# Performance work log

Hardware: AMD Instinct MI355X
Metric: run time of the kernel (lower is better)

Reference implementation:

```python
import jax, jax.numpy as jnp
import numpy as np

HID = 2880
NQ = 64
NKV = 8
HD = 64
THETA = 150000.0
WINDOW = 128
S = 8192


def _rope(x, positions):
    # x: [S, H, D]; half-split (rotate_half) convention
    d = x.shape[-1]
    inv_freq = 1.0 / (THETA ** (jnp.arange(0, d, 2, dtype=jnp.float32) / d))  # [D/2]
    ang = positions.astype(jnp.float32)[:, None] * inv_freq[None, :]          # [S, D/2]
    cos = jnp.cos(ang)[:, None, :]
    sin = jnp.sin(ang)[:, None, :]
    x1, x2 = jnp.split(x, 2, axis=-1)
    return jnp.concatenate([x1 * cos - x2 * sin, x2 * cos + x1 * sin], axis=-1)


def setup_inputs() -> dict:
    key = jax.random.key(0)
    ks = jax.random.split(key, 12)
    sd = 0.02
    return {
        "hidden": jax.random.normal(ks[0], (S, HID), dtype=jnp.float32),
        "positions": jnp.arange(S, dtype=jnp.int64) if jax.config.jax_enable_x64 else jnp.arange(S, dtype=jnp.int32),
        "Wq": jax.random.normal(ks[1], (HID, NQ * HD), dtype=jnp.float32) * sd,
        "bq": jax.random.normal(ks[2], (NQ * HD,), dtype=jnp.float32) * sd,
        "Wk": jax.random.normal(ks[3], (HID, NKV * HD), dtype=jnp.float32) * sd,
        "bk": jax.random.normal(ks[4], (NKV * HD,), dtype=jnp.float32) * sd,
        "Wv": jax.random.normal(ks[5], (HID, NKV * HD), dtype=jnp.float32) * sd,
        "bv": jax.random.normal(ks[6], (NKV * HD,), dtype=jnp.float32) * sd,
        "Wo": jax.random.normal(ks[7], (NQ * HD, HID), dtype=jnp.float32) * sd,
        "bo": jax.random.normal(ks[8], (HID,), dtype=jnp.float32) * sd,
    }


def _attention(hidden, positions, Wq, bq, Wk, bk, Wv, bv, Wo, bo):
    n_tok = hidden.shape[0]
    q = (hidden @ Wq + bq).reshape(n_tok, NQ, HD)
    k = (hidden @ Wk + bk).reshape(n_tok, NKV, HD)
    v = (hidden @ Wv + bv).reshape(n_tok, NKV, HD)
    q = _rope(q, positions)
    k = _rope(k, positions)

    # Blocked sliding-window causal attention (window == block size W).
    W = WINDOW
    nb = n_tok // W
    group = NQ // NKV
    qb = q.reshape(nb, W, NQ, HD)
    kb = k.reshape(nb, W, NKV, HD)
    vb = v.reshape(nb, W, NKV, HD)
    # each query block attends to its own block plus the previous one (2W keys)
    k_prev = jnp.concatenate([jnp.zeros_like(kb[:1]), kb[:-1]], axis=0)
    v_prev = jnp.concatenate([jnp.zeros_like(vb[:1]), vb[:-1]], axis=0)
    k_ctx = jnp.concatenate([k_prev, kb], axis=1)   # [nb, 2W, NKV, HD]
    v_ctx = jnp.concatenate([v_prev, vb], axis=1)
    # GQA: repeat KV heads to match query heads
    k_ctx = jnp.repeat(k_ctx, group, axis=2)        # [nb, 2W, NQ, HD]
    v_ctx = jnp.repeat(v_ctx, group, axis=2)

    scale = 1.0 / np.sqrt(HD)
    scores = jnp.einsum('bqhd,bkhd->bhqk', qb, k_ctx) * scale  # [nb, NQ, W, 2W]

    qi = jnp.arange(W)[:, None]            # local query pos
    ki = jnp.arange(2 * W)[None, :]        # local key pos within context
    diff = qi - ki + W                     # i - j (global)
    band = (diff >= 0) & (diff < WINDOW)   # causal + window
    kpos = jnp.arange(nb)[:, None, None] * W + ki[None] - W  # global key pos
    mask = band[None] & (kpos >= 0)        # [nb, W, 2W]

    neg = jnp.finfo(scores.dtype).min
    scores = jnp.where(mask[:, None, :, :], scores, neg)
    p = jax.nn.softmax(scores, axis=-1)
    attn = jnp.einsum('bhqk,bkhd->bqhd', p, v_ctx)  # [nb, W, NQ, HD]
    attn = attn.reshape(n_tok, NQ * HD)
    return attn @ Wo + bo


def reference(hidden, positions, Wq, bq, Wk, bk, Wv, bv, Wo, bo):
    return _attention(hidden, positions, Wq, bq, Wk, bk, Wv, bv, Wo, bo)
```

## Files before the change

kernel.cpp:

```cpp
#include <hip/hip_runtime.h>
#include <stdint.h>

#define S_TOK 8192
#define HID 2880
#define NQ 64
#define NKV 8
#define HD 64
#define QKV_N 5120
#define NO_PAD 2944

typedef __attribute__((ext_vector_type(8))) __bf16 bf16x8;
typedef __attribute__((ext_vector_type(4))) float f32x4;
typedef __attribute__((ext_vector_type(16))) float f32x16;

__device__ __forceinline__ unsigned short f2bf(float f) {
  unsigned int u = __builtin_bit_cast(unsigned int, f);
  u += 0x7fff + ((u >> 16) & 1);
  return (unsigned short)(u >> 16);
}
__device__ __forceinline__ float bf2f(unsigned short h) {
  unsigned int u = ((unsigned int)h) << 16;
  return __builtin_bit_cast(float, u);
}

__device__ __forceinline__ void async_lds16(const void* g, void* l) {
  __builtin_amdgcn_global_load_lds(
      (const __attribute__((address_space(1))) unsigned int*)g,
      (__attribute__((address_space(3))) unsigned int*)l, 16, 0, 0);
}

__global__ __launch_bounds__(256) void cvt_bf16_kernel(
    const float* __restrict__ src, unsigned short* __restrict__ dst) {
  size_t i = ((size_t)blockIdx.x * 256 + threadIdx.x) * 8;
  float4 a = *(const float4*)(src + i);
  float4 b = *(const float4*)(src + i + 4);
  union { unsigned short u[8]; uint4 v; } o;
  o.u[0] = f2bf(a.x); o.u[1] = f2bf(a.y); o.u[2] = f2bf(a.z); o.u[3] = f2bf(a.w);
  o.u[4] = f2bf(b.x); o.u[5] = f2bf(b.y); o.u[6] = f2bf(b.z); o.u[7] = f2bf(b.w);
  *(uint4*)(dst + i) = o.v;
}

__global__ __launch_bounds__(256) void transpose_cvt(
    const float* __restrict__ src, unsigned short* __restrict__ dst,
    int R, int C, int rowOff) {
  __shared__ float tile[32][33];
  int tx = threadIdx.x, ty = threadIdx.y;
  int c0 = blockIdx.x * 32, r0 = blockIdx.y * 32;
#pragma unroll
  for (int i = 0; i < 4; ++i)
    tile[ty + i * 8][tx] = src[(size_t)(r0 + ty + i * 8) * C + c0 + tx];
  __syncthreads();
#pragma unroll
  for (int i = 0; i < 4; ++i)
    dst[(size_t)(c0 + ty + i * 8 + rowOff) * R + r0 + tx] = f2bf(tile[tx][ty + i * 8]);
}

__global__ __launch_bounds__(256) void rope_kernel(
    unsigned short* __restrict__ qkv, const int* __restrict__ positions) {
  int gid = blockIdx.x * 256 + threadIdx.x;
  int d = gid & 31;
  int rest = gid >> 5;
  int head = rest % 72;
  int t = rest / 72;
  unsigned short* p = qkv + (size_t)t * QKV_N + head * 64;
  float x1 = bf2f(p[d]);
  float x2 = bf2f(p[d + 32]);
  float pos = (float)positions[t];
  float inv = exp2f(-0.5373313430f * (float)d);
  float ang = pos * inv;
  float s = sinf(ang), c = cosf(ang);
  p[d] = f2bf(x1 * c - x2 * s);
  p[d + 32] = f2bf(x2 * c + x1 * s);
}

template <int MODE>
__global__ __launch_bounds__(256) void gemm_bt(
    const unsigned short* __restrict__ A, const unsigned short* __restrict__ BT,
    void* __restrict__ Cout, int K,
    const float* __restrict__ b0, const float* __restrict__ b1,
    const float* __restrict__ b2) {
  __shared__ unsigned short lds[128 * 128];
  unsigned short* As = lds;
  unsigned short* Bs = lds + 128 * 64;
  const int tid = threadIdx.x;
  const int wave = tid >> 6, lane = tid & 63;
  const int l31 = lane & 31, lh = lane >> 5;
  const int wy = wave >> 1, wx = wave & 1;
  const int m0 = blockIdx.y * 128, n0 = blockIdx.x * 128;

  f32x16 acc[2][2];
#pragma unroll
  for (int i = 0; i < 2; ++i)
#pragma unroll
    for (int j = 0; j < 2; ++j)
#pragma unroll
      for (int r = 0; r < 16; ++r) acc[i][j][r] = 0.f;

  for (int k0 = 0; k0 < K; k0 += 64) {
    const unsigned short* Ag = A + (size_t)m0 * K + k0;
    const unsigned short* Bg = BT + (size_t)n0 * K + k0;
#pragma unroll
    for (int i = 0; i < 4; ++i) {
      int s = tid + i * 256;
      int row = s >> 3;
      int c = (s & 7) ^ (row & 7);
      async_lds16(Ag + (size_t)row * K + c * 8, &As[s * 8]);
      async_lds16(Bg + (size_t)row * K + c * 8, &Bs[s * 8]);
    }
    __syncthreads();
#pragma unroll
    for (int ks = 0; ks < 4; ++ks) {
      bf16x8 af[2], bfr[2];
#pragma unroll
      for (int ra = 0; ra < 2; ++ra) {
        int row = wy * 64 + ra * 32 + l31;
        int p = (ks * 2 + lh) ^ (row & 7);
        af[ra] = *(const bf16x8*)&As[row * 64 + p * 8];
      }
#pragma unroll
      for (int cb = 0; cb < 2; ++cb) {
        int row = wx * 64 + cb * 32 + l31;
        int p = (ks * 2 + lh) ^ (row & 7);
        bfr[cb] = *(const bf16x8*)&Bs[row * 64 + p * 8];
      }
#pragma unroll
      for (int ra = 0; ra < 2; ++ra)
#pragma unroll
        for (int cb = 0; cb < 2; ++cb)
          acc[ra][cb] = __builtin_amdgcn_mfma_f32_32x32x16_bf16(
              af[ra], bfr[cb], acc[ra][cb], 0, 0, 0);
    }
    __syncthreads();
  }

  if (MODE == 0) {
#pragma unroll
    for (int cb = 0; cb < 2; ++cb) {
      int col = wx * 64 + cb * 32 + l31;
      int gcol = n0 + col;
      float bias = (gcol < 4096) ? b0[gcol]
                                 : (gcol < 4608 ? b1[gcol - 4096] : b2[gcol - 4608]);
#pragma unroll
      for (int ra = 0; ra < 2; ++ra) {
#pragma unroll
        for (int r = 0; r < 16; ++r) {
          int row = wy * 64 + ra * 32 + (r & 3) + 8 * (r >> 2) + 4 * lh;
          lds[row * 128 + col] = f2bf(acc[ra][cb][r] + bias);
        }
      }
    }
    __syncthreads();
    unsigned short* C16 = (unsigned short*)Cout;
#pragma unroll
    for (int i = 0; i < 8; ++i) {
      int s = tid + i * 256;
      int row = s >> 4, cc = (s & 15) * 8;
      *(uint4*)(C16 + (size_t)(m0 + row) * QKV_N + n0 + cc) =
          *(const uint4*)&lds[row * 128 + cc];
    }
  } else {
#pragma unroll
    for (int cb = 0; cb < 2; ++cb) {
      int gcol = n0 + wx * 64 + cb * 32 + l31;
      if (gcol < HID) {
        float bias = b0[gcol];
#pragma unroll
        for (int ra = 0; ra < 2; ++ra) {
#pragma unroll
          for (int r = 0; r < 16; ++r) {
            int row = m0 + wy * 64 + ra * 32 + (r & 3) + 8 * (r >> 2) + 4 * lh;
            ((float*)Cout)[(size_t)row * HID + gcol] = acc[ra][cb][r] + bias;
          }
        }
      }
    }
  }
}

__global__ __launch_bounds__(256) void attn_kernel(
    const unsigned short* __restrict__ qkv, unsigned short* __restrict__ attn) {
  __shared__ unsigned short Qs[64 * 72];
  __shared__ unsigned short Ks[192 * 72];
  __shared__ unsigned short VTs[64 * 200];

  const int tid = threadIdx.x;
  const int B = blockIdx.x;
  const int h = blockIdx.y;
  const int hk = h >> 3;
  const int wave = tid >> 6, lane = tid & 63;
  const int quad = lane >> 4, ml = lane & 15;

#pragma unroll
  for (int it = 0; it < 2; ++it) {
    int s = tid + it * 256;
    int row = s >> 3, c = (s & 7) << 3;
    *(uint4*)&Qs[row * 72 + c] =
        *(const uint4*)(qkv + (size_t)(B * 64 + row) * QKV_N + h * 64 + c);
  }
#pragma unroll
  for (int it = 0; it < 6; ++it) {
    int s = tid + it * 256;
    int j = s >> 3, c = (s & 7) << 3;
    int tk = B * 64 - 128 + j;
    uint4 kv = make_uint4(0, 0, 0, 0), vv = make_uint4(0, 0, 0, 0);
    if (tk >= 0) {
      kv = *(const uint4*)(qkv + (size_t)tk * QKV_N + 4096 + hk * 64 + c);
      vv = *(const uint4*)(qkv + (size_t)tk * QKV_N + 4608 + hk * 64 + c);
    }
    *(uint4*)&Ks[j * 72 + c] = kv;
    union { uint4 q; unsigned short u[8]; } vu;
    vu.q = vv;
#pragma unroll
    for (int e = 0; e < 8; ++e) VTs[(c + e) * 200 + j] = vu.u[e];
  }
  __syncthreads();

  f32x4 zero = {0.f, 0.f, 0.f, 0.f};
  f32x4 sc[12];
#pragma unroll
  for (int jn = 0; jn < 12; ++jn) sc[jn] = zero;
#pragma unroll
  for (int kk = 0; kk < 2; ++kk) {
    bf16x8 af = *(const bf16x8*)&Qs[(wave * 16 + ml) * 72 + kk * 32 + quad * 8];
#pragma unroll
    for (int jn = 0; jn < 12; ++jn) {
      bf16x8 bfr = *(const bf16x8*)&Ks[(jn * 16 + ml) * 72 + kk * 32 + quad * 8];
      sc[jn] = __builtin_amdgcn_mfma_f32_16x16x32_bf16(af, bfr, sc[jn], 0, 0, 0);
    }
  }

  const float NEG = -3.0e38f;
  float mx[4], sm[4];
#pragma unroll
  for (int r = 0; r < 4; ++r) mx[r] = NEG;
#pragma unroll
  for (int jn = 0; jn < 12; ++jn) {
    int j = jn * 16 + ml;
#pragma unroll
    for (int r = 0; r < 4; ++r) {
      int i = wave * 16 + quad * 4 + r;
      bool valid = (j > i) && (j <= i + 128) && (B * 64 + j - 128 >= 0);
      float v = valid ? sc[jn][r] * 0.125f : NEG;
      sc[jn][r] = v;
      mx[r] = fmaxf(mx[r], v);
    }
  }
#pragma unroll
  for (int r = 0; r < 4; ++r) {
#pragma unroll
    for (int off = 1; off < 16; off <<= 1)
      mx[r] = fmaxf(mx[r], __shfl_xor(mx[r], off, 64));
    sm[r] = 0.f;
  }
#pragma unroll
  for (int jn = 0; jn < 12; ++jn) {
#pragma unroll
    for (int r = 0; r < 4; ++r) {
      float p = expf(sc[jn][r] - mx[r]);
      sc[jn][r] = p;
      sm[r] += p;
    }
  }
#pragma unroll
  for (int r = 0; r < 4; ++r) {
#pragma unroll
    for (int off = 1; off < 16; off <<= 1) sm[r] += __shfl_xor(sm[r], off, 64);
    sm[r] = 1.0f / sm[r];
  }
  __syncthreads();

  unsigned short* P = Ks;
#pragma unroll
  for (int jn = 0; jn < 12; ++jn) {
#pragma unroll
    for (int r = 0; r < 4; ++r)
      P[(wave * 16 + quad * 4 + r) * 200 + jn * 16 + ml] = f2bf(sc[jn][r] * sm[r]);
  }
  __syncthreads();

  f32x4 ov[4];
#pragma unroll
  for (int jn = 0; jn < 4; ++jn) ov[jn] = zero;
#pragma unroll
  for (int ks = 0; ks < 6; ++ks) {
    bf16x8 af = *(const bf16x8*)&P[(wave * 16 + ml) * 200 + ks * 32 + quad * 8];
#pragma unroll
    for (int jn = 0; jn < 4; ++jn) {
      bf16x8 bfr = *(const bf16x8*)&VTs[(jn * 16 + ml) * 200 + ks * 32 + quad * 8];
      ov[jn] = __builtin_amdgcn_mfma_f32_16x16x32_bf16(af, bfr, ov[jn], 0, 0, 0);
    }
  }
#pragma unroll
  for (int jn = 0; jn < 4; ++jn) {
#pragma unroll
    for (int r = 0; r < 4; ++r) {
      int row = B * 64 + wave * 16 + quad * 4 + r;
      attn[(size_t)row * 4096 + h * 64 + jn * 16 + ml] = f2bf(ov[jn][r]);
    }
  }
}

extern "C" void kernel_launch(void* const* d_in, const int* in_sizes, int n_in,
                              void* d_out, int out_size, void* d_ws, size_t ws_size,
                              hipStream_t stream) {
  const float* hidden = (const float*)d_in[0];
  const int* positions = (const int*)d_in[1];
  const float* Wq = (const float*)d_in[2];
  const float* bq = (const float*)d_in[3];
  const float* Wk = (const float*)d_in[4];
  const float* bk = (const float*)d_in[5];
  const float* Wv = (const float*)d_in[6];
  const float* bv = (const float*)d_in[7];
  const float* Wo = (const float*)d_in[8];
  const float* bo = (const float*)d_in[9];
  float* out = (float*)d_out;

  char* ws = (char*)d_ws;
  unsigned short* A_h   = (unsigned short*)(ws);
  unsigned short* BTqkv = (unsigned short*)(ws + 47185920);
  unsigned short* qkv   = (unsigned short*)(ws + 76677120);
  unsigned short* BTo   = (unsigned short*)(ws + 160563200);
  unsigned short* attn  = (unsigned short*)(ws);

  cvt_bf16_kernel<<<11520, 256, 0, stream>>>(hidden, A_h);
  dim3 tb(32, 8);
  transpose_cvt<<<dim3(128, 90), tb, 0, stream>>>(Wq, BTqkv, HID, 4096, 0);
  transpose_cvt<<<dim3(16, 90), tb, 0, stream>>>(Wk, BTqkv, HID, 512, 4096);
  transpose_cvt<<<dim3(16, 90), tb, 0, stream>>>(Wv, BTqkv, HID, 512, 4608);
  transpose_cvt<<<dim3(90, 128), tb, 0, stream>>>(Wo, BTo, 4096, HID, 0);
  hipMemsetAsync(BTo + (size_t)HID * 4096, 0, (size_t)(NO_PAD - HID) * 4096 * 2, stream);

  gemm_bt<0><<<dim3(QKV_N / 128, S_TOK / 128), 256, 0, stream>>>(
      A_h, BTqkv, qkv, HID, bq, bk, bv);
  rope_kernel<<<73728, 256, 0, stream>>>(qkv, positions);
  attn_kernel<<<dim3(S_TOK / 64, NQ), 256, 0, stream>>>(qkv, attn);
  gemm_bt<1><<<dim3(NO_PAD / 128, S_TOK / 128), 256, 0, stream>>>(
      attn, BTo, out, 4096, bo, nullptr, nullptr);
}
```

Before: 969.7 us.

## Fuse RoPE into QKV GEMM epilogue, swizzle LDS writes, coalesce attention output

Removes the standalone rope kernel and applies the rotation inside the QKV GEMM epilogue, which saves a full read-modify-write pass over the q/k part of the qkv buffer. The epilogue LDS stores get an XOR swizzle to reduce bank conflicts. The V transpose in the attention kernel uses a lane-rotated element order for the same reason. Attention output is staged through LDS so global writes become coalesced 16-byte stores, and the GEMM gets a launch_bounds occupancy hint that may raise register pressure.

```diff
diff --git a/kernel.cpp b/kernel.cpp
--- a/kernel.cpp
+++ b/kernel.cpp
@@ -55,30 +55,12 @@
     dst[(size_t)(c0 + ty + i * 8 + rowOff) * R + r0 + tx] = f2bf(tile[tx][ty + i * 8]);
 }
 
-__global__ __launch_bounds__(256) void rope_kernel(
-    unsigned short* __restrict__ qkv, const int* __restrict__ positions) {
-  int gid = blockIdx.x * 256 + threadIdx.x;
-  int d = gid & 31;
-  int rest = gid >> 5;
-  int head = rest % 72;
-  int t = rest / 72;
-  unsigned short* p = qkv + (size_t)t * QKV_N + head * 64;
-  float x1 = bf2f(p[d]);
-  float x2 = bf2f(p[d + 32]);
-  float pos = (float)positions[t];
-  float inv = exp2f(-0.5373313430f * (float)d);
-  float ang = pos * inv;
-  float s = sinf(ang), c = cosf(ang);
-  p[d] = f2bf(x1 * c - x2 * s);
-  p[d + 32] = f2bf(x2 * c + x1 * s);
-}
-
 template <int MODE>
-__global__ __launch_bounds__(256) void gemm_bt(
+__global__ __launch_bounds__(256, 5) void gemm_bt(
     const unsigned short* __restrict__ A, const unsigned short* __restrict__ BT,
     void* __restrict__ Cout, int K,
     const float* __restrict__ b0, const float* __restrict__ b1,
-    const float* __restrict__ b2) {
+    const float* __restrict__ b2, const int* __restrict__ positions) {
   __shared__ unsigned short lds[128 * 128];
   unsigned short* As = lds;
   unsigned short* Bs = lds + 128 * 64;
@@ -134,19 +116,32 @@
   }
 
   if (MODE == 0) {
-#pragma unroll
-    for (int cb = 0; cb < 2; ++cb) {
-      int col = wx * 64 + cb * 32 + l31;
-      int gcol = n0 + col;
-      float bias = (gcol < 4096) ? b0[gcol]
-                                 : (gcol < 4608 ? b1[gcol - 4096] : b2[gcol - 4608]);
-#pragma unroll
-      for (int ra = 0; ra < 2; ++ra) {
-#pragma unroll
-        for (int r = 0; r < 16; ++r) {
-          int row = wy * 64 + ra * 32 + (r & 3) + 8 * (r >> 2) + 4 * lh;
-          lds[row * 128 + col] = f2bf(acc[ra][cb][r] + bias);
+    const bool doRope = (n0 < 4608);
+    const float inv = exp2f(-0.5373313430f * (float)l31);
+    const int gcol0 = n0 + wx * 64 + l31;
+    const int gcol1 = gcol0 + 32;
+    const float bias0 = (gcol0 < 4096) ? b0[gcol0]
+                                       : (gcol0 < 4608 ? b1[gcol0 - 4096] : b2[gcol0 - 4608]);
+    const float bias1 = (gcol1 < 4096) ? b0[gcol1]
+                                       : (gcol1 < 4608 ? b1[gcol1 - 4096] : b2[gcol1 - 4608]);
+    const int colbase = wx * 64 + l31;
+#pragma unroll
+    for (int ra = 0; ra < 2; ++ra) {
+#pragma unroll
+      for (int r = 0; r < 16; ++r) {
+        int lrow = wy * 64 + ra * 32 + (r & 3) + 8 * (r >> 2) + 4 * lh;
+        float x1 = acc[ra][0][r] + bias0;
+        float x2 = acc[ra][1][r] + bias1;
+        float o1 = x1, o2 = x2;
+        if (doRope) {
+          float ang = (float)positions[m0 + lrow] * inv;
+          float s = sinf(ang), c = cosf(ang);
+          o1 = x1 * c - x2 * s;
+          o2 = x2 * c + x1 * s;
         }
+        int swz = ((lrow >> 2) & 1) << 5;
+        lds[lrow * 128 + (colbase ^ swz)] = f2bf(o1);
+        lds[lrow * 128 + ((colbase + 32) ^ swz)] = f2bf(o2);
       }
     }
     __syncthreads();
@@ -155,8 +150,9 @@
     for (int i = 0; i < 8; ++i) {
       int s = tid + i * 256;
       int row = s >> 4, cc = (s & 15) * 8;
+      int pcc = cc ^ (((row >> 2) & 1) << 5);
       *(uint4*)(C16 + (size_t)(m0 + row) * QKV_N + n0 + cc) =
-          *(const uint4*)&lds[row * 128 + cc];
+          *(const uint4*)&lds[row * 128 + pcc];
     }
   } else {
 #pragma unroll
@@ -189,6 +185,7 @@
   const int hk = h >> 3;
   const int wave = tid >> 6, lane = tid & 63;
   const int quad = lane >> 4, ml = lane & 15;
+  const int r7 = lane & 7;
 
 #pragma unroll
   for (int it = 0; it < 2; ++it) {
@@ -208,10 +205,23 @@
       vv = *(const uint4*)(qkv + (size_t)tk * QKV_N + 4608 + hk * 64 + c);
     }
     *(uint4*)&Ks[j * 72 + c] = kv;
-    union { uint4 q; unsigned short u[8]; } vu;
-    vu.q = vv;
-#pragma unroll
-    for (int e = 0; e < 8; ++e) VTs[(c + e) * 200 + j] = vu.u[e];
+    unsigned int a0 = vv.x, a1 = vv.y, a2 = vv.z, a3 = vv.w;
+    int rd = (r7 >> 1) & 3;
+    unsigned int b0 = (rd & 2) ? a2 : a0, b1 = (rd & 2) ? a3 : a1;
+    unsigned int b2 = (rd & 2) ? a0 : a2, b3 = (rd & 2) ? a1 : a3;
+    unsigned int d0 = (rd & 1) ? b1 : b0, d1 = (rd & 1) ? b2 : b1;
+    unsigned int d2 = (rd & 1) ? b3 : b2, d3 = (rd & 1) ? b0 : b3;
+    bool oddr = (r7 & 1);
+    unsigned int e0 = oddr ? ((d0 >> 16) | (d1 << 16)) : d0;
+    unsigned int e1 = oddr ? ((d1 >> 16) | (d2 << 16)) : d1;
+    unsigned int e2 = oddr ? ((d2 >> 16) | (d3 << 16)) : d2;
+    unsigned int e3 = oddr ? ((d3 >> 16) | (d0 << 16)) : d3;
+    unsigned int rw[4] = {e0, e1, e2, e3};
+#pragma unroll
+    for (int i = 0; i < 8; ++i) {
+      int e = (i + r7) & 7;
+      VTs[(c + e) * 200 + j] = (unsigned short)(rw[i >> 1] >> ((i & 1) * 16));
+    }
   }
   __syncthreads();
 
@@ -290,13 +300,20 @@
       ov[jn] = __builtin_amdgcn_mfma_f32_16x16x32_bf16(af, bfr, ov[jn], 0, 0, 0);
     }
   }
+  __syncthreads();
 #pragma unroll
   for (int jn = 0; jn < 4; ++jn) {
 #pragma unroll
-    for (int r = 0; r < 4; ++r) {
-      int row = B * 64 + wave * 16 + quad * 4 + r;
-      attn[(size_t)row * 4096 + h * 64 + jn * 16 + ml] = f2bf(ov[jn][r]);
-    }
+    for (int r = 0; r < 4; ++r)
+      Qs[(wave * 16 + quad * 4 + r) * 72 + jn * 16 + ml] = f2bf(ov[jn][r]);
+  }
+  __syncthreads();
+#pragma unroll
+  for (int it = 0; it < 2; ++it) {
+    int s = tid + it * 256;
+    int row = s >> 3, cc = (s & 7) * 8;
+    *(uint4*)(attn + (size_t)(B * 64 + row) * 4096 + h * 64 + cc) =
+        *(const uint4*)&Qs[row * 72 + cc];
   }
 }
 
@@ -331,9 +348,8 @@
   hipMemsetAsync(BTo + (size_t)HID * 4096, 0, (size_t)(NO_PAD - HID) * 4096 * 2, stream);
 
   gemm_bt<0><<<dim3(QKV_N / 128, S_TOK / 128), 256, 0, stream>>>(
-      A_h, BTqkv, qkv, HID, bq, bk, bv);
-  rope_kernel<<<73728, 256, 0, stream>>>(qkv, positions);
+      A_h, BTqkv, qkv, HID, bq, bk, bv, positions);
   attn_kernel<<<dim3(S_TOK / 64, NQ), 256, 0, stream>>>(qkv, attn);
   gemm_bt<1><<<dim3(NO_PAD / 128, S_TOK / 128), 256, 0, stream>>>(
-      attn, BTo, out, 4096, bo, nullptr, nullptr);
-}
+      attn, BTo, out, 4096, bo, nullptr, nullptr, nullptr);
+}
```

Result: slower. 1.193 ms (+23.0%).
